# Kernel tuning notes

Hardware: AMD Instinct MI355X
Metric: run time of the kernel (lower is better)

Reference implementation:

```python
import jax, jax.numpy as jnp
import numpy as np

B, S, H, K = 4, 4096, 2048, 4
EPS = 1e-6

def rmsnorm(x, w, eps=EPS):
    xf = x.astype(jnp.float32)
    var = jnp.mean(xf * xf, axis=-1, keepdims=True)
    return (w * (xf * jax.lax.rsqrt(var + eps)).astype(x.dtype))

def setup_inputs() -> dict:
    key = jax.random.key(0)
    k1, k2, k3 = jax.random.split(key, 3)
    hidden_states = jax.random.normal(k1, (B, S, H), dtype=jnp.float32)
    norm_weight = jnp.ones((H,), dtype=jnp.float32)
    conv_weight = jax.random.normal(k2, (H, 1, K), dtype=jnp.float32) * 0.1
    conv_bias = jax.random.normal(k3, (H,), dtype=jnp.float32) * 0.1
    return {"hidden_states": hidden_states, "norm_weight": norm_weight,
            "conv_weight": conv_weight, "conv_bias": conv_bias}

def reference(hidden_states, norm_weight, conv_weight, conv_bias):
    # RMSNorm over hidden dim
    x = rmsnorm(hidden_states, norm_weight)          # [B, S, H]
    x = jnp.transpose(x, (0, 2, 1))                  # [B, H, S] (NCH)
    # Depthwise causal conv1d: left-pad K-1 so output length == S
    y = jax.lax.conv_general_dilated(
        x, conv_weight,                              # [H, 1, K] (OIH), groups=H
        window_strides=(1,),
        padding=[(K - 1, 0)],
        dimension_numbers=("NCH", "OIH", "NCH"),
        feature_group_count=H,
    )                                                # [B, H, S]
    y = y + conv_bias[None, :, None]
    return jnp.transpose(y, (0, 2, 1))               # [B, S, H]
```

## Files before the change

kernel.cpp:

```cpp
#include <hip/hip_runtime.h>


#define BQ 4
#define SQ 4096
#define HQ 2048
#define KQ 4
#define TROWS 32
#define NTHREADS 512
#define NWAVES (NTHREADS / 64)

__global__ __launch_bounds__(NTHREADS, 2) void ttt_conv_kernel(
    const float* __restrict__ x,
    const float* __restrict__ nw,
    const float* __restrict__ cw,
    const float* __restrict__ cb,
    float* __restrict__ out)
{
    __shared__ float part[2][NWAVES];

    const int tid  = threadIdx.x;
    const int lane = tid & 63;
    const int wid  = tid >> 6;

    const int tilesPerB = SQ / TROWS;
    const int b  = blockIdx.x / tilesPerB;
    const int s0 = (blockIdx.x % tilesPerB) * TROWS;
    const int h4 = tid * 4;

    const float4 w4    = *reinterpret_cast<const float4*>(nw + h4);
    const float4 bias4 = *reinterpret_cast<const float4*>(cb + h4);
    const float4 r0 = *reinterpret_cast<const float4*>(cw + (size_t)(h4 + 0) * KQ);
    const float4 r1 = *reinterpret_cast<const float4*>(cw + (size_t)(h4 + 1) * KQ);
    const float4 r2 = *reinterpret_cast<const float4*>(cw + (size_t)(h4 + 2) * KQ);
    const float4 r3 = *reinterpret_cast<const float4*>(cw + (size_t)(h4 + 3) * KQ);
    const float4 cw0 = make_float4(r0.x, r1.x, r2.x, r3.x);
    const float4 cw1 = make_float4(r0.y, r1.y, r2.y, r3.y);
    const float4 cw2 = make_float4(r0.z, r1.z, r2.z, r3.z);
    const float4 cw3 = make_float4(r0.w, r1.w, r2.w, r3.w);

    const float* xb = x   + (size_t)b * SQ * HQ + h4;
    float*       ob = out + (size_t)b * SQ * HQ + h4;

    float4 win0 = make_float4(0, 0, 0, 0);
    float4 win1 = make_float4(0, 0, 0, 0);
    float4 win2 = make_float4(0, 0, 0, 0);
    float4 win3 = make_float4(0, 0, 0, 0);

    const int sEnd = s0 + TROWS;
    int s = s0 - (KQ - 1);

    float4 xv_next = make_float4(0, 0, 0, 0);
    if (s >= 0) xv_next = *reinterpret_cast<const float4*>(xb + (size_t)s * HQ);

    int parity = 0;
    for (; s < sEnd; ++s) {
        const float4 xv = xv_next;
        const int sn = s + 1;
        if (sn < sEnd) {
            xv_next = (sn >= 0)
                ? *reinterpret_cast<const float4*>(xb + (size_t)sn * HQ)
                : make_float4(0, 0, 0, 0);
        }

        float p = xv.x * xv.x + xv.y * xv.y + xv.z * xv.z + xv.w * xv.w;
        #pragma unroll
        for (int off = 32; off >= 1; off >>= 1)
            p += __shfl_xor(p, off, 64);
        if (lane == 0) part[parity][wid] = p;
        __syncthreads();
        float tot = 0.f;
        #pragma unroll
        for (int wv = 0; wv < NWAVES; ++wv) tot += part[parity][wv];
        parity ^= 1;

        const float scale = rsqrtf(tot * (1.0f / HQ) + 1e-6f);

        float4 xn;
        xn.x = xv.x * scale * w4.x;
        xn.y = xv.y * scale * w4.y;
        xn.z = xv.z * scale * w4.z;
        xn.w = xv.w * scale * w4.w;

        win0 = win1; win1 = win2; win2 = win3; win3 = xn;

        if (s >= s0) {
            float4 o;
            o.x = bias4.x + cw0.x * win0.x + cw1.x * win1.x + cw2.x * win2.x + cw3.x * win3.x;
            o.y = bias4.y + cw0.y * win0.y + cw1.y * win1.y + cw2.y * win2.y + cw3.y * win3.y;
            o.z = bias4.z + cw0.z * win0.z + cw1.z * win1.z + cw2.z * win2.z + cw3.z * win3.z;
            o.w = bias4.w + cw0.w * win0.w + cw1.w * win1.w + cw2.w * win2.w + cw3.w * win3.w;
            *reinterpret_cast<float4*>(ob + (size_t)s * HQ) = o;
        }
    }
}

extern "C" void kernel_launch(void* const* d_in, const int* in_sizes, int n_in,
                              void* d_out, int out_size, void* d_ws, size_t ws_size,
                              hipStream_t stream) {
    const float* x  = (const float*)d_in[0];
    const float* nw = (const float*)d_in[1];
    const float* cw = (const float*)d_in[2];
    const float* cb = (const float*)d_in[3];
    float* o = (float*)d_out;

    const int grid = BQ * (SQ / TROWS);
    ttt_conv_kernel<<<grid, NTHREADS, 0, stream>>>(x, nw, cw, cb, o);
}
```

Before: 244.3 us.

## Batch RMS reductions four rows per barrier with grouped prefetch and nontemporal stores

Processes rows in groups of four: loads four rows ahead, does the wave shuffles and shared-memory partial sums for all four at once, and needs only one block barrier per group instead of one per row. This cuts barrier and latency stalls and raises memory-level parallelism. It also raises the launch-bounds occupancy hint and writes the output with nontemporal stores to avoid polluting the cache. In exchange it adds register pressure and one extra halo row of reads per tile.

Result: no change. 241.8 us (-1.0%).

```diff
diff --git a/kernel.cpp b/kernel.cpp
--- a/kernel.cpp
+++ b/kernel.cpp
@@ -6,17 +6,21 @@
 #define HQ 2048
 #define KQ 4
 #define TROWS 32
+#define RB 4
+#define NGRP (TROWS / RB + 1)
 #define NTHREADS 512
 #define NWAVES (NTHREADS / 64)
 
-__global__ __launch_bounds__(NTHREADS, 2) void ttt_conv_kernel(
+typedef float f32x4 __attribute__((ext_vector_type(4)));
+
+__global__ __launch_bounds__(NTHREADS, 4) void ttt_conv_kernel(
     const float* __restrict__ x,
-    const float* __restrict__ nw,
-    const float* __restrict__ cw,
-    const float* __restrict__ cb,
+    const float* __restrict__ gamma,
+    const float* __restrict__ cwp,
+    const float* __restrict__ cbp,
     float* __restrict__ out)
 {
-    __shared__ float part[2][NWAVES];
+    __shared__ float part[2][RB][NWAVES];
 
     const int tid  = threadIdx.x;
     const int lane = tid & 63;
@@ -27,69 +31,97 @@
     const int s0 = (blockIdx.x % tilesPerB) * TROWS;
     const int h4 = tid * 4;
 
-    const float4 w4    = *reinterpret_cast<const float4*>(nw + h4);
-    const float4 bias4 = *reinterpret_cast<const float4*>(cb + h4);
-    const float4 r0 = *reinterpret_cast<const float4*>(cw + (size_t)(h4 + 0) * KQ);
-    const float4 r1 = *reinterpret_cast<const float4*>(cw + (size_t)(h4 + 1) * KQ);
-    const float4 r2 = *reinterpret_cast<const float4*>(cw + (size_t)(h4 + 2) * KQ);
-    const float4 r3 = *reinterpret_cast<const float4*>(cw + (size_t)(h4 + 3) * KQ);
-    const float4 cw0 = make_float4(r0.x, r1.x, r2.x, r3.x);
-    const float4 cw1 = make_float4(r0.y, r1.y, r2.y, r3.y);
-    const float4 cw2 = make_float4(r0.z, r1.z, r2.z, r3.z);
-    const float4 cw3 = make_float4(r0.w, r1.w, r2.w, r3.w);
+    const float4 g4    = *reinterpret_cast<const float4*>(gamma + h4);
+    const float4 bias4 = *reinterpret_cast<const float4*>(cbp + h4);
+    const float4 r0 = *reinterpret_cast<const float4*>(cwp + (size_t)(h4 + 0) * KQ);
+    const float4 r1 = *reinterpret_cast<const float4*>(cwp + (size_t)(h4 + 1) * KQ);
+    const float4 r2 = *reinterpret_cast<const float4*>(cwp + (size_t)(h4 + 2) * KQ);
+    const float4 r3 = *reinterpret_cast<const float4*>(cwp + (size_t)(h4 + 3) * KQ);
+    const float4 c0 = make_float4(r0.x, r1.x, r2.x, r3.x);
+    const float4 c1 = make_float4(r0.y, r1.y, r2.y, r3.y);
+    const float4 c2 = make_float4(r0.z, r1.z, r2.z, r3.z);
+    const float4 c3 = make_float4(r0.w, r1.w, r2.w, r3.w);
 
     const float* xb = x   + (size_t)b * SQ * HQ + h4;
     float*       ob = out + (size_t)b * SQ * HQ + h4;
 
-    float4 win0 = make_float4(0, 0, 0, 0);
-    float4 win1 = make_float4(0, 0, 0, 0);
-    float4 win2 = make_float4(0, 0, 0, 0);
-    float4 win3 = make_float4(0, 0, 0, 0);
+    const float4 f4z = make_float4(0.f, 0.f, 0.f, 0.f);
+    float4 wm3 = f4z, wm2 = f4z, wm1 = f4z;
 
-    const int sEnd = s0 + TROWS;
-    int s = s0 - (KQ - 1);
+    float4 buf[RB];
+    {
+        const int base = s0 - RB;
+        #pragma unroll
+        for (int r = 0; r < RB; ++r) {
+            const int s = base + r;
+            buf[r] = (s >= 0) ? *reinterpret_cast<const float4*>(xb + (size_t)s * HQ)
+                              : f4z;
+        }
+    }
 
-    float4 xv_next = make_float4(0, 0, 0, 0);
-    if (s >= 0) xv_next = *reinterpret_cast<const float4*>(xb + (size_t)s * HQ);
+    for (int g = 0; g < NGRP; ++g) {
+        const int base = s0 - RB + g * RB;
 
-    int parity = 0;
-    for (; s < sEnd; ++s) {
-        const float4 xv = xv_next;
-        const int sn = s + 1;
-        if (sn < sEnd) {
-            xv_next = (sn >= 0)
-                ? *reinterpret_cast<const float4*>(xb + (size_t)sn * HQ)
-                : make_float4(0, 0, 0, 0);
+        float4 cur[RB];
+        #pragma unroll
+        for (int r = 0; r < RB; ++r) cur[r] = buf[r];
+
+        float p[RB];
+        #pragma unroll
+        for (int r = 0; r < RB; ++r)
+            p[r] = cur[r].x * cur[r].x + cur[r].y * cur[r].y
+                 + cur[r].z * cur[r].z + cur[r].w * cur[r].w;
+
+        if (g + 1 < NGRP) {
+            const int nb = base + RB;
+            #pragma unroll
+            for (int r = 0; r < RB; ++r) {
+                const int s = nb + r;
+                buf[r] = (s >= 0) ? *reinterpret_cast<const float4*>(xb + (size_t)s * HQ)
+                                  : f4z;
+            }
         }
 
-        float p = xv.x * xv.x + xv.y * xv.y + xv.z * xv.z + xv.w * xv.w;
         #pragma unroll
-        for (int off = 32; off >= 1; off >>= 1)
-            p += __shfl_xor(p, off, 64);
-        if (lane == 0) part[parity][wid] = p;
+        for (int off = 32; off >= 1; off >>= 1) {
+            #pragma unroll
+            for (int r = 0; r < RB; ++r)
+                p[r] += __shfl_xor(p[r], off, 64);
+        }
+        if (lane == 0) {
+            #pragma unroll
+            for (int r = 0; r < RB; ++r) part[g & 1][r][wid] = p[r];
+        }
         __syncthreads();
-        float tot = 0.f;
+
+        float tot[RB];
         #pragma unroll
-        for (int wv = 0; wv < NWAVES; ++wv) tot += part[parity][wv];
-        parity ^= 1;
+        for (int r = 0; r < RB; ++r) {
+            const float4 pa = *reinterpret_cast<const float4*>(&part[g & 1][r][0]);
+            const float4 pb = *reinterpret_cast<const float4*>(&part[g & 1][r][4]);
+            tot[r] = (pa.x + pa.y + pa.z + pa.w) + (pb.x + pb.y + pb.z + pb.w);
+        }
 
-        const float scale = rsqrtf(tot * (1.0f / HQ) + 1e-6f);
+        #pragma unroll
+        for (int r = 0; r < RB; ++r) {
+            const float scale = rsqrtf(tot[r] * (1.0f / HQ) + 1e-6f);
+            float4 xn;
+            xn.x = cur[r].x * scale * g4.x;
+            xn.y = cur[r].y * scale * g4.y;
+            xn.z = cur[r].z * scale * g4.z;
+            xn.w = cur[r].w * scale * g4.w;
 
-        float4 xn;
-        xn.x = xv.x * scale * w4.x;
-        xn.y = xv.y * scale * w4.y;
-        xn.z = xv.z * scale * w4.z;
-        xn.w = xv.w * scale * w4.w;
-
-        win0 = win1; win1 = win2; win2 = win3; win3 = xn;
-
-        if (s >= s0) {
-            float4 o;
-            o.x = bias4.x + cw0.x * win0.x + cw1.x * win1.x + cw2.x * win2.x + cw3.x * win3.x;
-            o.y = bias4.y + cw0.y * win0.y + cw1.y * win1.y + cw2.y * win2.y + cw3.y * win3.y;
-            o.z = bias4.z + cw0.z * win0.z + cw1.z * win1.z + cw2.z * win2.z + cw3.z * win3.z;
-            o.w = bias4.w + cw0.w * win0.w + cw1.w * win1.w + cw2.w * win2.w + cw3.w * win3.w;
-            *reinterpret_cast<float4*>(ob + (size_t)s * HQ) = o;
+            if (g > 0) {
+                f32x4 o;
+                o.x = bias4.x + c0.x * wm3.x + c1.x * wm2.x + c2.x * wm1.x + c3.x * xn.x;
+                o.y = bias4.y + c0.y * wm3.y + c1.y * wm2.y + c2.y * wm1.y + c3.y * xn.y;
+                o.z = bias4.z + c0.z * wm3.z + c1.z * wm2.z + c2.z * wm1.z + c3.z * xn.z;
+                o.w = bias4.w + c0.w * wm3.w + c1.w * wm2.w + c2.w * wm1.w + c3.w * xn.w;
+                const int s = base + r;
+                __builtin_nontemporal_store(
+                    o, reinterpret_cast<f32x4*>(ob + (size_t)s * HQ));
+            }
+            wm3 = wm2; wm2 = wm1; wm1 = xn;
         }
     }
 }
```
